# Kernel tuning notes

Measured on AMD Instinct MI355X. Metric: run time of the kernel, lower is better.

Reference implementation:

```python
import jax, jax.numpy as jnp
import numpy as np

B, S, E = 2, 2048, 1024
H, G = 16, 4
HS = E // H          # head size = 64
SCALE = HS ** -0.5


def setup_inputs() -> dict:
    key = jax.random.key(0)
    ks = jax.random.split(key, 6)
    sd = 0.02
    return {
        "x": jax.random.normal(ks[0], (B, S, E), dtype=jnp.float32),
        "Wq": jax.random.normal(ks[1], (E, E), dtype=jnp.float32) * sd,
        "Wk": jax.random.normal(ks[2], (HS * G, E), dtype=jnp.float32) * sd,
        "Wv": jax.random.normal(ks[3], (HS * G, E), dtype=jnp.float32) * sd,
        "Wo": jax.random.normal(ks[4], (E, E), dtype=jnp.float32) * sd,
        "bo": jnp.zeros((E,), dtype=jnp.float32),
    }


def reference(x, Wq, Wk, Wv, Wo, bo):
    b, s, e = x.shape
    # projections (nn.Linear: y = x @ W.T)
    q = (x @ Wq.T).reshape(b, s, H, HS).transpose(0, 2, 1, 3)      # [b,H,s,hs]
    k = (x @ Wk.T).reshape(b, s, G, HS).transpose(0, 2, 1, 3)      # [b,G,s,hs]
    v = (x @ Wv.T).reshape(b, s, G, HS).transpose(0, 2, 1, 3)      # [b,G,s,hs]
    # expand KV groups to heads (group-major, matching torch expand/reshape)
    rep = H // G
    k = jnp.repeat(k, rep, axis=1)                                  # [b,H,s,hs]
    v = jnp.repeat(v, rep, axis=1)                                  # [b,H,s,hs]
    scores = SCALE * jnp.einsum("bhqd,bhkd->bhqk", q, k)           # [b,H,s,s]
    weights = jax.nn.softmax(scores, axis=-1)                       # dropout = identity (eval)
    attn = jnp.einsum("bhqk,bhkd->bhqd", weights, v)               # [b,H,s,hs]
    attn = attn.transpose(0, 2, 1, 3).reshape(b, s, e)              # [b,s,E]
    return attn @ Wo.T + bo
```

## Files before the change

### kernel.cpp

```cpp
#include <hip/hip_runtime.h>


typedef __bf16 bf16_t;
typedef __bf16 bf16x8 __attribute__((ext_vector_type(8)));
typedef __bf16 bf16x4 __attribute__((ext_vector_type(4)));
typedef short s16x4 __attribute__((ext_vector_type(4)));
typedef float f32x4 __attribute__((ext_vector_type(4)));

#define B_ 2
#define S_ 2048
#define E_ 1024
#define H_ 16
#define G_ 4
#define HS_ 64
#define SCALE_ 0.125f

#define CX_  0u
#define CWQ_ 4194304u
#define CWK_ 5242880u
#define CWV_ 5505024u
#define CWO_ 5767168u
#define CEND_ 6815744u

__device__ inline f32x4 mfma32(bf16x8 a, bf16x8 b, f32x4 c) {
  return __builtin_amdgcn_mfma_f32_16x16x32_bf16(a, b, c, 0, 0, 0);
}

#if __has_builtin(__builtin_amdgcn_mfma_f32_16x16x16bf16_1k)
__device__ inline f32x4 mfma_pv(s16x4 a, s16x4 b, f32x4 c) {
  return __builtin_amdgcn_mfma_f32_16x16x16bf16_1k(a, b, c, 0, 0, 0);
}
#else
__device__ inline f32x4 mfma_pv(s16x4 a, s16x4 b, f32x4 c) {
  asm volatile("s_nop 2\n\tv_mfma_f32_16x16x16_bf16 %0, %1, %2, %0\n\t"
               "s_nop 7\n\ts_nop 3"
               : "+v"(c) : "v"(a), "v"(b));
  return c;
}
#endif

__global__ __launch_bounds__(256) void cvt5(
    const float* __restrict__ x, const float* __restrict__ wq,
    const float* __restrict__ wk, const float* __restrict__ wv,
    const float* __restrict__ wo, bf16_t* __restrict__ dst) {
  const unsigned i = ((unsigned)blockIdx.x * 256u + threadIdx.x) * 8u;
  const float* src;
  unsigned off;
  if (i < CWQ_)      { src = x;  off = CX_;  }
  else if (i < CWK_) { src = wq; off = CWQ_; }
  else if (i < CWV_) { src = wk; off = CWK_; }
  else if (i < CWO_) { src = wv; off = CWV_; }
  else               { src = wo; off = CWO_; }
  const float4* p = (const float4*)(src + (i - off));
  float4 a = p[0], b = p[1];
  bf16x8 v;
  v[0] = (bf16_t)a.x; v[1] = (bf16_t)a.y; v[2] = (bf16_t)a.z; v[3] = (bf16_t)a.w;
  v[4] = (bf16_t)b.x; v[5] = (bf16_t)b.y; v[6] = (bf16_t)b.z; v[7] = (bf16_t)b.w;
  *(bf16x8*)(dst + i) = v;
}

__global__ __launch_bounds__(256) void qkv_proj(
    const bf16_t* __restrict__ X, const bf16_t* __restrict__ Wq,
    const bf16_t* __restrict__ Wk, const bf16_t* __restrict__ Wv,
    bf16_t* __restrict__ Qw, bf16_t* __restrict__ Kw, bf16_t* __restrict__ Vw) {
  __shared__ alignas(16) bf16_t As[64 * 64];
  __shared__ alignas(16) bf16_t Bs[128 * 64];
  const int tid = threadIdx.x;
  const int lane = tid & 63;
  const int wvi = tid >> 6;
  const int quad = lane >> 4, l15 = lane & 15;
  const int wm = wvi >> 1, wn = wvi & 1;

  const int mt = blockIdx.x / 12;
  const int nt = blockIdx.x % 12;

  const bf16_t* Wbase;
  int nLoc, mode;
  if (nt < 8)       { Wbase = Wq; nLoc = nt * 128;        mode = 0; }
  else if (nt < 10) { Wbase = Wk; nLoc = (nt - 8) * 128;  mode = 1; }
  else              { Wbase = Wv; nLoc = (nt - 10) * 128; mode = 2; }

  const int sr = tid >> 3;
  const int sc = tid & 7;
  const bf16_t* Ag = X + (size_t)(mt * 64) * 1024;
  const bf16_t* Bg = Wbase + (size_t)nLoc * 1024;

  f32x4 acc[2][4] = {};

  for (int k0 = 0; k0 < 1024; k0 += 64) {
    bf16x8 ta[2], tb[4];
#pragma unroll
    for (int j = 0; j < 2; ++j)
      ta[j] = *(const bf16x8*)(Ag + (size_t)(j * 32 + sr) * 1024 + k0 + sc * 8);
#pragma unroll
    for (int j = 0; j < 4; ++j)
      tb[j] = *(const bf16x8*)(Bg + (size_t)(j * 32 + sr) * 1024 + k0 + sc * 8);
#pragma unroll
    for (int j = 0; j < 2; ++j) {
      const int r = j * 32 + sr;
      *(bf16x8*)&As[r * 64 + ((sc ^ (r & 7)) * 8)] = ta[j];
    }
#pragma unroll
    for (int j = 0; j < 4; ++j) {
      const int r = j * 32 + sr;
      *(bf16x8*)&Bs[r * 64 + ((sc ^ (r & 7)) * 8)] = tb[j];
    }
    __syncthreads();
#pragma unroll
    for (int ks = 0; ks < 2; ++ks) {
      bf16x8 a[2], b[4];
#pragma unroll
      for (int i = 0; i < 2; ++i) {
        const int r = wm * 32 + i * 16 + l15;
        a[i] = *(const bf16x8*)&As[r * 64 + (((ks * 4 + quad) ^ (r & 7)) * 8)];
      }
#pragma unroll
      for (int j = 0; j < 4; ++j) {
        const int r = wn * 64 + j * 16 + l15;
        b[j] = *(const bf16x8*)&Bs[r * 64 + (((ks * 4 + quad) ^ (r & 7)) * 8)];
      }
#pragma unroll
      for (int i = 0; i < 2; ++i)
#pragma unroll
        for (int j = 0; j < 4; ++j) acc[i][j] = mfma32(a[i], b[j], acc[i][j]);
    }
    __syncthreads();
  }

#pragma unroll
  for (int i = 0; i < 2; ++i)
#pragma unroll
    for (int rr = 0; rr < 4; ++rr) {
      const int row = mt * 64 + wm * 32 + i * 16 + quad * 4 + rr;
      const int bb = row >> 11, s = row & 2047;
#pragma unroll
      for (int j = 0; j < 4; ++j) {
        const int cl = nLoc + wn * 64 + j * 16 + l15;
        const float v = acc[i][j][rr];
        if (mode == 0)
          Qw[((size_t)((bb * H_ + (cl >> 6)) * S_ + s)) * HS_ + (cl & 63)] = (bf16_t)v;
        else if (mode == 1)
          Kw[((size_t)((bb * G_ + (cl >> 6)) * S_ + s)) * HS_ + (cl & 63)] = (bf16_t)v;
        else
          Vw[(size_t)(bb * G_ + (cl >> 6)) * S_ * HS_ + (s >> 4) * (HS_ * 16) +
             (cl & 63) * 16 + (s & 15)] = (bf16_t)v;
      }
    }
}

__global__ __launch_bounds__(256, 2) void attn_fwd(
    const bf16_t* __restrict__ Q, const bf16_t* __restrict__ K,
    const bf16_t* __restrict__ V16, bf16_t* __restrict__ A) {
  __shared__ float Ml[2][64 * 69];
  const int tid = threadIdx.x;
  const int lane = tid & 63;
  const int wvi = tid >> 6;
  const int pairIdx = wvi >> 1;
  const int half = wvi & 1;
  const int quad = lane >> 4, l15 = lane & 15;

  const int pair = blockIdx.x * 2 + pairIdx;
  const int qt = pair & 127;
  const int g = (pair >> 7) & 3;
  const int b = pair >> 9;

  const bf16_t* Kp =
      K + (size_t)(b * G_ + g) * S_ * HS_ + (size_t)half * 1024 * HS_;
  const bf16_t* Vp =
      V16 + (size_t)(b * G_ + g) * S_ * HS_ + (size_t)half * 1024 * HS_;

  bf16x8 qf[4][2];
#pragma unroll
  for (int hh = 0; hh < 4; ++hh) {
    const bf16_t* Qp =
        Q + ((size_t)((b * H_ + g * 4 + hh) * S_ + qt * 16)) * HS_;
    bf16x8 r0 = *(const bf16x8*)(Qp + (size_t)l15 * HS_ + quad * 8);
    bf16x8 r1 = *(const bf16x8*)(Qp + (size_t)l15 * HS_ + 32 + quad * 8);
#pragma unroll
    for (int e = 0; e < 8; ++e) {
      qf[hh][0][e] = (bf16_t)((float)r0[e] * SCALE_);
      qf[hh][1][e] = (bf16_t)((float)r1[e] * SCALE_);
    }
  }

  f32x4 o[4][4] = {};
  float lacc[4] = {0.0f, 0.0f, 0.0f, 0.0f};

  const bf16_t* kc = Kp;
  const bf16_t* vc = Vp;
  bf16x8 ka0 = *(const bf16x8*)(kc + (size_t)l15 * HS_ + quad * 8);
  bf16x8 ka1 = *(const bf16x8*)(kc + (size_t)l15 * HS_ + 32 + quad * 8);
  bf16x4 vb[4];
#pragma unroll
  for (int t = 0; t < 4; ++t)
    vb[t] = *(const bf16x4*)(vc + (t * 16 + l15) * 16 + quad * 4);

  for (int it = 0; it < 64; ++it) {
    const bf16_t* kn = kc + 1024;
    const bf16_t* vn = vc + 1024;
    bf16x8 nka0 = *(const bf16x8*)(kn + (size_t)l15 * HS_ + quad * 8);
    bf16x8 nka1 = *(const bf16x8*)(kn + (size_t)l15 * HS_ + 32 + quad * 8);
    bf16x4 nvb[4];
#pragma unroll
    for (int t = 0; t < 4; ++t)
      nvb[t] = *(const bf16x4*)(vn + (t * 16 + l15) * 16 + quad * 4);

#pragma unroll
    for (int hh = 0; hh < 4; ++hh) {
      f32x4 sc = {};
      sc = mfma32(ka0, qf[hh][0], sc);
      sc = mfma32(ka1, qf[hh][1], sc);
      bf16x4 pb;
      float ps = 0.0f;
#pragma unroll
      for (int r = 0; r < 4; ++r) {
        float p = __expf(sc[r]);
        ps += p;
        pb[r] = (bf16_t)p;
      }
      lacc[hh] += ps;
      const s16x4 pa = __builtin_bit_cast(s16x4, pb);
#pragma unroll
      for (int t = 0; t < 4; ++t)
        o[hh][t] = mfma_pv(pa, __builtin_bit_cast(s16x4, vb[t]), o[hh][t]);
    }

    ka0 = nka0; ka1 = nka1;
#pragma unroll
    for (int t = 0; t < 4; ++t) vb[t] = nvb[t];
    kc = kn; vc = vn;
  }

  float* ml = &Ml[pairIdx][lane * 69];
  if (half == 1) {
#pragma unroll
    for (int hh = 0; hh < 4; ++hh) {
#pragma unroll
      for (int t = 0; t < 4; ++t)
#pragma unroll
        for (int r = 0; r < 4; ++r) ml[hh * 16 + t * 4 + r] = o[hh][t][r];
      ml[64 + hh] = lacc[hh];
    }
  }
  __syncthreads();
  if (half == 0) {
#pragma unroll
    for (int hh = 0; hh < 4; ++hh) {
#pragma unroll
      for (int t = 0; t < 4; ++t)
#pragma unroll
        for (int r = 0; r < 4; ++r) o[hh][t][r] += ml[hh * 16 + t * 4 + r];
      lacc[hh] += ml[64 + hh];
    }

#pragma unroll
    for (int hh = 0; hh < 4; ++hh) {
      float l = lacc[hh];
      l += __shfl_xor(l, 16, 64);
      l += __shfl_xor(l, 32, 64);
      float linv[4];
#pragma unroll
      for (int r = 0; r < 4; ++r)
        linv[r] = 1.0f / __shfl(l, quad * 4 + r, 64);
#pragma unroll
      for (int t = 0; t < 4; ++t)
#pragma unroll
        for (int r = 0; r < 4; ++r) {
          const int row = qt * 16 + quad * 4 + r;
          A[((size_t)(b * S_ + row)) * E_ + (g * 4 + hh) * HS_ + t * 16 + l15] =
              (bf16_t)(o[hh][t][r] * linv[r]);
        }
    }
  }
}

__global__ __launch_bounds__(256) void out_proj(
    const bf16_t* __restrict__ Aw, const bf16_t* __restrict__ Wo,
    const float* __restrict__ bias, float* __restrict__ out) {
  __shared__ alignas(16) bf16_t As[64 * 64];
  __shared__ alignas(16) bf16_t Bs[128 * 64];
  const int tid = threadIdx.x;
  const int lane = tid & 63;
  const int wvi = tid >> 6;
  const int quad = lane >> 4, l15 = lane & 15;
  const int wm = wvi >> 1, wn = wvi & 1;

  const int mt = blockIdx.x >> 3;
  const int nt = blockIdx.x & 7;

  const int sr = tid >> 3;
  const int sc = tid & 7;
  const bf16_t* Ag = Aw + (size_t)(mt * 64) * 1024;
  const bf16_t* Bg = Wo + (size_t)(nt * 128) * 1024;

  f32x4 acc[2][4] = {};

  for (int k0 = 0; k0 < 1024; k0 += 64) {
    bf16x8 ta[2], tb[4];
#pragma unroll
    for (int j = 0; j < 2; ++j)
      ta[j] = *(const bf16x8*)(Ag + (size_t)(j * 32 + sr) * 1024 + k0 + sc * 8);
#pragma unroll
    for (int j = 0; j < 4; ++j)
      tb[j] = *(const bf16x8*)(Bg + (size_t)(j * 32 + sr) * 1024 + k0 + sc * 8);
#pragma unroll
    for (int j = 0; j < 2; ++j) {
      const int r = j * 32 + sr;
      *(bf16x8*)&As[r * 64 + ((sc ^ (r & 7)) * 8)] = ta[j];
    }
#pragma unroll
    for (int j = 0; j < 4; ++j) {
      const int r = j * 32 + sr;
      *(bf16x8*)&Bs[r * 64 + ((sc ^ (r & 7)) * 8)] = tb[j];
    }
    __syncthreads();
#pragma unroll
    for (int ks = 0; ks < 2; ++ks) {
      bf16x8 a[2], b[4];
#pragma unroll
      for (int i = 0; i < 2; ++i) {
        const int r = wm * 32 + i * 16 + l15;
        a[i] = *(const bf16x8*)&As[r * 64 + (((ks * 4 + quad) ^ (r & 7)) * 8)];
      }
#pragma unroll
      for (int j = 0; j < 4; ++j) {
        const int r = wn * 64 + j * 16 + l15;
        b[j] = *(const bf16x8*)&Bs[r * 64 + (((ks * 4 + quad) ^ (r & 7)) * 8)];
      }
#pragma unroll
      for (int i = 0; i < 2; ++i)
#pragma unroll
        for (int j = 0; j < 4; ++j) acc[i][j] = mfma32(a[i], b[j], acc[i][j]);
    }
    __syncthreads();
  }

#pragma unroll
  for (int i = 0; i < 2; ++i)
#pragma unroll
    for (int j = 0; j < 4; ++j)
#pragma unroll
      for (int rr = 0; rr < 4; ++rr) {
        const int row = mt * 64 + wm * 32 + i * 16 + quad * 4 + rr;
        const int col = nt * 128 + wn * 64 + j * 16 + l15;
        out[(size_t)row * 1024 + col] = acc[i][j][rr] + bias[col];
      }
}

extern "C" void kernel_launch(void* const* d_in, const int* in_sizes, int n_in,
                              void* d_out, int out_size, void* d_ws, size_t ws_size,
                              hipStream_t stream) {
  const float* x  = (const float*)d_in[0];
  const float* Wq = (const float*)d_in[1];
  const float* Wk = (const float*)d_in[2];
  const float* Wv = (const float*)d_in[3];
  const float* Wo = (const float*)d_in[4];
  const float* bo = (const float*)d_in[5];
  float* out = (float*)d_out;

  bf16_t* ws = (bf16_t*)d_ws;
  bf16_t* Xb  = ws + CX_;
  bf16_t* Wqb = ws + CWQ_;
  bf16_t* Wkb = ws + CWK_;
  bf16_t* Wvb = ws + CWV_;
  bf16_t* Wob = ws + CWO_;
  bf16_t* Qw = ws + CEND_;
  bf16_t* Kw = Qw + (size_t)B_ * H_ * S_ * HS_;
  bf16_t* Vw = Kw + (size_t)B_ * G_ * S_ * HS_;
  bf16_t* Aw = Vw + (size_t)B_ * G_ * HS_ * S_;

  cvt5<<<CEND_ / 2048, 256, 0, stream>>>(x, Wq, Wk, Wv, Wo, ws);
  qkv_proj<<<768, 256, 0, stream>>>(Xb, Wqb, Wkb, Wvb, Qw, Kw, Vw);
  attn_fwd<<<512, 256, 0, stream>>>(Qw, Kw, Vw, Aw);
  out_proj<<<512, 256, 0, stream>>>(Aw, Wob, bo, out);
}
```

Baseline: 173.6 us.

## Split attention KV range across four waves per block and use exp2

Each block now handles one query tile/group with four waves, each covering a quarter of the key sequence, and the partial outputs are merged by a two-level shared-memory tree reduction. The grid doubles to 1024 blocks and launch bounds allow four blocks per CU, which raises parallelism and occupancy. The K/V loads are double-buffered with an explicit two-stage unrolled loop. Softmax uses exp2 with the log2(e) factor folded into the Q scaling. The cost is extra reduction passes and syncthreads, plus register pressure from the higher occupancy target. As in the original, no running max is subtracted before exponentiation.

```diff
diff --git a/kernel.cpp b/kernel.cpp
--- a/kernel.cpp
+++ b/kernel.cpp
@@ -14,6 +14,7 @@
 #define G_ 4
 #define HS_ 64
 #define SCALE_ 0.125f
+#define SL2E_ 0.1803368801111244f
 
 #define CX_  0u
 #define CWQ_ 4194304u
@@ -37,6 +38,12 @@
                : "+v"(c) : "v"(a), "v"(b));
   return c;
 }
+#endif
+
+#if __has_builtin(__builtin_amdgcn_exp2f)
+__device__ inline float fexp2(float x) { return __builtin_amdgcn_exp2f(x); }
+#else
+__device__ inline float fexp2(float x) { return exp2f(x); }
 #endif
 
 __global__ __launch_bounds__(256) void cvt5(
@@ -148,26 +155,24 @@
     }
 }
 
-__global__ __launch_bounds__(256, 2) void attn_fwd(
+__global__ __launch_bounds__(256, 4) void attn_fwd(
     const bf16_t* __restrict__ Q, const bf16_t* __restrict__ K,
     const bf16_t* __restrict__ V16, bf16_t* __restrict__ A) {
   __shared__ float Ml[2][64 * 69];
   const int tid = threadIdx.x;
   const int lane = tid & 63;
   const int wvi = tid >> 6;
-  const int pairIdx = wvi >> 1;
-  const int half = wvi & 1;
   const int quad = lane >> 4, l15 = lane & 15;
 
-  const int pair = blockIdx.x * 2 + pairIdx;
-  const int qt = pair & 127;
-  const int g = (pair >> 7) & 3;
-  const int b = pair >> 9;
+  const int unit = blockIdx.x;
+  const int qt = unit & 127;
+  const int g = (unit >> 7) & 3;
+  const int b = unit >> 9;
 
   const bf16_t* Kp =
-      K + (size_t)(b * G_ + g) * S_ * HS_ + (size_t)half * 1024 * HS_;
+      K + (size_t)(b * G_ + g) * S_ * HS_ + (size_t)wvi * 512 * HS_;
   const bf16_t* Vp =
-      V16 + (size_t)(b * G_ + g) * S_ * HS_ + (size_t)half * 1024 * HS_;
+      V16 + (size_t)(b * G_ + g) * S_ * HS_ + (size_t)wvi * 512 * HS_;
 
   bf16x8 qf[4][2];
 #pragma unroll
@@ -178,61 +183,63 @@
     bf16x8 r1 = *(const bf16x8*)(Qp + (size_t)l15 * HS_ + 32 + quad * 8);
 #pragma unroll
     for (int e = 0; e < 8; ++e) {
-      qf[hh][0][e] = (bf16_t)((float)r0[e] * SCALE_);
-      qf[hh][1][e] = (bf16_t)((float)r1[e] * SCALE_);
+      qf[hh][0][e] = (bf16_t)((float)r0[e] * SL2E_);
+      qf[hh][1][e] = (bf16_t)((float)r1[e] * SL2E_);
     }
   }
 
   f32x4 o[4][4] = {};
   float lacc[4] = {0.0f, 0.0f, 0.0f, 0.0f};
 
+  auto loadK = [&](const bf16_t* kc, bf16x8& a0, bf16x8& a1) {
+    a0 = *(const bf16x8*)(kc + (size_t)l15 * HS_ + quad * 8);
+    a1 = *(const bf16x8*)(kc + (size_t)l15 * HS_ + 32 + quad * 8);
+  };
+  auto loadV = [&](const bf16_t* vc, bf16x4* vb) {
+#pragma unroll
+    for (int t = 0; t < 4; ++t)
+      vb[t] = *(const bf16x4*)(vc + (t * 16 + l15) * 16 + quad * 4);
+  };
+  auto compute = [&](bf16x8 a0, bf16x8 a1, const bf16x4* vb) {
+#pragma unroll
+    for (int hh = 0; hh < 4; ++hh) {
+      f32x4 sc = {};
+      sc = mfma32(a0, qf[hh][0], sc);
+      sc = mfma32(a1, qf[hh][1], sc);
+      bf16x4 pb;
+      float ps = 0.0f;
+#pragma unroll
+      for (int r = 0; r < 4; ++r) {
+        float p = fexp2(sc[r]);
+        ps += p;
+        pb[r] = (bf16_t)p;
+      }
+      lacc[hh] += ps;
+      const s16x4 pa = __builtin_bit_cast(s16x4, pb);
+#pragma unroll
+      for (int t = 0; t < 4; ++t)
+        o[hh][t] = mfma_pv(pa, __builtin_bit_cast(s16x4, vb[t]), o[hh][t]);
+    }
+  };
+
+  bf16x8 kaA0, kaA1, kaB0, kaB1;
+  bf16x4 vbA[4], vbB[4];
   const bf16_t* kc = Kp;
   const bf16_t* vc = Vp;
-  bf16x8 ka0 = *(const bf16x8*)(kc + (size_t)l15 * HS_ + quad * 8);
-  bf16x8 ka1 = *(const bf16x8*)(kc + (size_t)l15 * HS_ + 32 + quad * 8);
-  bf16x4 vb[4];
-#pragma unroll
-  for (int t = 0; t < 4; ++t)
-    vb[t] = *(const bf16x4*)(vc + (t * 16 + l15) * 16 + quad * 4);
-
-  for (int it = 0; it < 64; ++it) {
-    const bf16_t* kn = kc + 1024;
-    const bf16_t* vn = vc + 1024;
-    bf16x8 nka0 = *(const bf16x8*)(kn + (size_t)l15 * HS_ + quad * 8);
-    bf16x8 nka1 = *(const bf16x8*)(kn + (size_t)l15 * HS_ + 32 + quad * 8);
-    bf16x4 nvb[4];
-#pragma unroll
-    for (int t = 0; t < 4; ++t)
-      nvb[t] = *(const bf16x4*)(vn + (t * 16 + l15) * 16 + quad * 4);
-
-#pragma unroll
-    for (int hh = 0; hh < 4; ++hh) {
-      f32x4 sc = {};
-      sc = mfma32(ka0, qf[hh][0], sc);
-      sc = mfma32(ka1, qf[hh][1], sc);
-      bf16x4 pb;
-      float ps = 0.0f;
-#pragma unroll
-      for (int r = 0; r < 4; ++r) {
-        float p = __expf(sc[r]);
-        ps += p;
-        pb[r] = (bf16_t)p;
-      }
-      lacc[hh] += ps;
-      const s16x4 pa = __builtin_bit_cast(s16x4, pb);
-#pragma unroll
-      for (int t = 0; t < 4; ++t)
-        o[hh][t] = mfma_pv(pa, __builtin_bit_cast(s16x4, vb[t]), o[hh][t]);
-    }
-
-    ka0 = nka0; ka1 = nka1;
-#pragma unroll
-    for (int t = 0; t < 4; ++t) vb[t] = nvb[t];
-    kc = kn; vc = vn;
-  }
-
-  float* ml = &Ml[pairIdx][lane * 69];
-  if (half == 1) {
+  loadK(kc, kaA0, kaA1);
+  loadV(vc, vbA);
+  for (int it = 0; it < 32; it += 2) {
+    loadK(kc + 1024, kaB0, kaB1);
+    loadV(vc + 1024, vbB);
+    compute(kaA0, kaA1, vbA);
+    loadK(kc + 2048, kaA0, kaA1);
+    loadV(vc + 2048, vbA);
+    compute(kaB0, kaB1, vbB);
+    kc += 2048; vc += 2048;
+  }
+
+  if (wvi == 1 || wvi == 3) {
+    float* ml = &Ml[wvi >> 1][lane * 69];
 #pragma unroll
     for (int hh = 0; hh < 4; ++hh) {
 #pragma unroll
@@ -243,7 +250,32 @@
     }
   }
   __syncthreads();
-  if (half == 0) {
+  if (wvi == 0 || wvi == 2) {
+    float* ml = &Ml[wvi >> 1][lane * 69];
+#pragma unroll
+    for (int hh = 0; hh < 4; ++hh) {
+#pragma unroll
+      for (int t = 0; t < 4; ++t)
+#pragma unroll
+        for (int r = 0; r < 4; ++r) o[hh][t][r] += ml[hh * 16 + t * 4 + r];
+      lacc[hh] += ml[64 + hh];
+    }
+  }
+  __syncthreads();
+  if (wvi == 2) {
+    float* ml = &Ml[0][lane * 69];
+#pragma unroll
+    for (int hh = 0; hh < 4; ++hh) {
+#pragma unroll
+      for (int t = 0; t < 4; ++t)
+#pragma unroll
+        for (int r = 0; r < 4; ++r) ml[hh * 16 + t * 4 + r] = o[hh][t][r];
+      ml[64 + hh] = lacc[hh];
+    }
+  }
+  __syncthreads();
+  if (wvi == 0) {
+    float* ml = &Ml[0][lane * 69];
 #pragma unroll
     for (int hh = 0; hh < 4; ++hh) {
 #pragma unroll
@@ -371,6 +403,6 @@
 
   cvt5<<<CEND_ / 2048, 256, 0, stream>>>(x, Wq, Wk, Wv, Wo, ws);
   qkv_proj<<<768, 256, 0, stream>>>(Xb, Wqb, Wkb, Wvb, Qw, Kw, Vw);
-  attn_fwd<<<512, 256, 0, stream>>>(Qw, Kw, Vw, Aw);
+  attn_fwd<<<1024, 256, 0, stream>>>(Qw, Kw, Vw, Aw);
   out_proj<<<512, 256, 0, stream>>>(Aw, Wob, bo, out);
 }
```

Measured after the change: 316.5 us. 82.4% more time.

## Use direct global-to-LDS loads in projection GEMMs and enlarge QKV M tile

Applied to the files above, without the earlier changes.

Both projection GEMMs now fill shared memory with global_load_lds 16-byte transfers that skip the register round-trip, and the XOR swizzle is dropped because those loads write LDS linearly. The QKV projection tile grows from 64x128 to 128x128, with each wave computing a 64x64 block, so the grid halves and each weight tile is reused across more rows. The cost is likely LDS bank conflicts on the unswizzled MFMA fragment reads, more accumulator registers, and fewer blocks in flight.

```diff
diff --git a/kernel.cpp b/kernel.cpp
--- a/kernel.cpp
+++ b/kernel.cpp
@@ -38,6 +38,12 @@
   return c;
 }
 #endif
+
+__device__ __forceinline__ void gl_lds16(const bf16_t* g, bf16_t* l) {
+  __builtin_amdgcn_global_load_lds(
+      (const __attribute__((address_space(1))) void*)(g),
+      (__attribute__((address_space(3))) void*)(l), 16, 0, 0);
+}
 
 __global__ __launch_bounds__(256) void cvt5(
     const float* __restrict__ x, const float* __restrict__ wq,
@@ -63,7 +69,7 @@
     const bf16_t* __restrict__ X, const bf16_t* __restrict__ Wq,
     const bf16_t* __restrict__ Wk, const bf16_t* __restrict__ Wv,
     bf16_t* __restrict__ Qw, bf16_t* __restrict__ Kw, bf16_t* __restrict__ Vw) {
-  __shared__ alignas(16) bf16_t As[64 * 64];
+  __shared__ alignas(16) bf16_t As[128 * 64];
   __shared__ alignas(16) bf16_t Bs[128 * 64];
   const int tid = threadIdx.x;
   const int lane = tid & 63;
@@ -82,45 +88,34 @@
 
   const int sr = tid >> 3;
   const int sc = tid & 7;
-  const bf16_t* Ag = X + (size_t)(mt * 64) * 1024;
+  const bf16_t* Ag = X + (size_t)(mt * 128) * 1024;
   const bf16_t* Bg = Wbase + (size_t)nLoc * 1024;
 
-  f32x4 acc[2][4] = {};
+  f32x4 acc[4][4] = {};
 
   for (int k0 = 0; k0 < 1024; k0 += 64) {
-    bf16x8 ta[2], tb[4];
-#pragma unroll
-    for (int j = 0; j < 2; ++j)
-      ta[j] = *(const bf16x8*)(Ag + (size_t)(j * 32 + sr) * 1024 + k0 + sc * 8);
-#pragma unroll
-    for (int j = 0; j < 4; ++j)
-      tb[j] = *(const bf16x8*)(Bg + (size_t)(j * 32 + sr) * 1024 + k0 + sc * 8);
-#pragma unroll
-    for (int j = 0; j < 2; ++j) {
-      const int r = j * 32 + sr;
-      *(bf16x8*)&As[r * 64 + ((sc ^ (r & 7)) * 8)] = ta[j];
-    }
 #pragma unroll
     for (int j = 0; j < 4; ++j) {
       const int r = j * 32 + sr;
-      *(bf16x8*)&Bs[r * 64 + ((sc ^ (r & 7)) * 8)] = tb[j];
+      gl_lds16(Ag + (size_t)r * 1024 + k0 + sc * 8, &As[r * 64 + sc * 8]);
+      gl_lds16(Bg + (size_t)r * 1024 + k0 + sc * 8, &Bs[r * 64 + sc * 8]);
     }
     __syncthreads();
 #pragma unroll
     for (int ks = 0; ks < 2; ++ks) {
-      bf16x8 a[2], b[4];
-#pragma unroll
-      for (int i = 0; i < 2; ++i) {
-        const int r = wm * 32 + i * 16 + l15;
-        a[i] = *(const bf16x8*)&As[r * 64 + (((ks * 4 + quad) ^ (r & 7)) * 8)];
+      bf16x8 a[4], b[4];
+#pragma unroll
+      for (int i = 0; i < 4; ++i) {
+        const int r = wm * 64 + i * 16 + l15;
+        a[i] = *(const bf16x8*)&As[r * 64 + (ks * 4 + quad) * 8];
       }
 #pragma unroll
       for (int j = 0; j < 4; ++j) {
         const int r = wn * 64 + j * 16 + l15;
-        b[j] = *(const bf16x8*)&Bs[r * 64 + (((ks * 4 + quad) ^ (r & 7)) * 8)];
-      }
-#pragma unroll
-      for (int i = 0; i < 2; ++i)
+        b[j] = *(const bf16x8*)&Bs[r * 64 + (ks * 4 + quad) * 8];
+      }
+#pragma unroll
+      for (int i = 0; i < 4; ++i)
 #pragma unroll
         for (int j = 0; j < 4; ++j) acc[i][j] = mfma32(a[i], b[j], acc[i][j]);
     }
@@ -128,10 +123,10 @@
   }
 
 #pragma unroll
-  for (int i = 0; i < 2; ++i)
+  for (int i = 0; i < 4; ++i)
 #pragma unroll
     for (int rr = 0; rr < 4; ++rr) {
-      const int row = mt * 64 + wm * 32 + i * 16 + quad * 4 + rr;
+      const int row = mt * 128 + wm * 64 + i * 16 + quad * 4 + rr;
       const int bb = row >> 11, s = row & 2047;
 #pragma unroll
       for (int j = 0; j < 4; ++j) {
@@ -296,22 +291,15 @@
   f32x4 acc[2][4] = {};
 
   for (int k0 = 0; k0 < 1024; k0 += 64) {
-    bf16x8 ta[2], tb[4];
-#pragma unroll
-    for (int j = 0; j < 2; ++j)
-      ta[j] = *(const bf16x8*)(Ag + (size_t)(j * 32 + sr) * 1024 + k0 + sc * 8);
-#pragma unroll
-    for (int j = 0; j < 4; ++j)
-      tb[j] = *(const bf16x8*)(Bg + (size_t)(j * 32 + sr) * 1024 + k0 + sc * 8);
 #pragma unroll
     for (int j = 0; j < 2; ++j) {
       const int r = j * 32 + sr;
-      *(bf16x8*)&As[r * 64 + ((sc ^ (r & 7)) * 8)] = ta[j];
+      gl_lds16(Ag + (size_t)r * 1024 + k0 + sc * 8, &As[r * 64 + sc * 8]);
     }
 #pragma unroll
     for (int j = 0; j < 4; ++j) {
       const int r = j * 32 + sr;
-      *(bf16x8*)&Bs[r * 64 + ((sc ^ (r & 7)) * 8)] = tb[j];
+      gl_lds16(Bg + (size_t)r * 1024 + k0 + sc * 8, &Bs[r * 64 + sc * 8]);
     }
     __syncthreads();
 #pragma unroll
@@ -320,12 +308,12 @@
 #pragma unroll
       for (int i = 0; i < 2; ++i) {
         const int r = wm * 32 + i * 16 + l15;
-        a[i] = *(const bf16x8*)&As[r * 64 + (((ks * 4 + quad) ^ (r & 7)) * 8)];
+        a[i] = *(const bf16x8*)&As[r * 64 + (ks * 4 + quad) * 8];
       }
 #pragma unroll
       for (int j = 0; j < 4; ++j) {
         const int r = wn * 64 + j * 16 + l15;
-        b[j] = *(const bf16x8*)&Bs[r * 64 + (((ks * 4 + quad) ^ (r & 7)) * 8)];
+        b[j] = *(const bf16x8*)&Bs[r * 64 + (ks * 4 + quad) * 8];
       }
 #pragma unroll
       for (int i = 0; i < 2; ++i)
@@ -370,7 +358,7 @@
   bf16_t* Aw = Vw + (size_t)B_ * G_ * HS_ * S_;
 
   cvt5<<<CEND_ / 2048, 256, 0, stream>>>(x, Wq, Wk, Wv, Wo, ws);
-  qkv_proj<<<768, 256, 0, stream>>>(Xb, Wqb, Wkb, Wvb, Qw, Kw, Vw);
+  qkv_proj<<<384, 256, 0, stream>>>(Xb, Wqb, Wkb, Wvb, Qw, Kw, Vw);
   attn_fwd<<<512, 256, 0, stream>>>(Qw, Kw, Vw, Aw);
   out_proj<<<512, 256, 0, stream>>>(Aw, Wob, bo, out);
 }
```

After: 185.7 us. 7.0% more time.
